# Kernel optimization log

Measured on AMD Instinct MI355X. Metric: run time of the kernel, lower is better.

The kernel has to match this reference:

```python
import jax, jax.numpy as jnp
import numpy as np

EPS = 1e-8
B, CIN, COUT, T, H, W = 16, 16, 64, 50, 32, 32
K = 3  # cubic kernel

# Surrogate-gradient Heaviside spike: forward = step(mthr > 0),
# backward = sigma * sigmoid'(sigma * mthr) (standard SurrogateHeaviside).
@jax.custom_vjp
def spike_fn(mthr, sigma):
    return (mthr > 0.0).astype(mthr.dtype)

def _spk_fwd(mthr, sigma):
    return spike_fn(mthr, sigma), (mthr, sigma)

def _spk_bwd(res, g):
    mthr, sigma = res
    sig = jax.nn.sigmoid(sigma * mthr)
    dsig = sig * (1.0 - sig)
    return (g * sigma * dsig, jnp.sum(g * mthr * dsig).reshape(sigma.shape))

spike_fn.defvjp(_spk_fwd, _spk_bwd)


def setup_inputs() -> dict:
    key = jax.random.key(0)
    k1, k2, k3 = jax.random.split(key, 3)
    x = jax.random.normal(k1, (B, CIN, T, H, W), dtype=jnp.float32)
    # torch init: normal(mean=0, std=w_init_std*sqrt(1/(in_ch*prod(kernel))))
    w = jax.random.normal(k2, (COUT, CIN, K, K, K), jnp.float32) * np.sqrt(1.0 / (CIN * K * K * K)).astype(np.float32)
    v = jax.random.normal(k3, (COUT, COUT), jnp.float32) * np.sqrt(1.0 / COUT).astype(np.float32)
    beta = jnp.full((1,), 0.85, jnp.float32)       # one_per_layer, constant init, clamped [0,1]
    b = jnp.ones((COUT,), jnp.float32)             # constant init 1.0, clamped >= 0
    sigma = jnp.full((1,), 10.0, jnp.float32)      # surrogate_sigma, 'one' mode
    return {"x": x, "w": w, "v": v, "beta": beta, "b": b, "sigma": sigma}


def reference(x, w, v, beta, b, sigma):
    # conv3d front-end, padding=ceil((k-1)*d/2)=1, then crop to output_shape (no-op here)
    conv_x = jax.lax.conv_general_dilated(
        x, w, window_strides=(1, 1, 1), padding=[(1, 1), (1, 1), (1, 1)],
        dimension_numbers=("NCDHW", "OIDHW", "NCDHW"))
    conv_x = conv_x[:, :, :, :H, :W]  # [B, COUT, T, H, W]

    d = jnp.einsum("abcde,fbcde->af", w, w)          # [COUT, COUT] lateral reset mixing
    norm = jnp.sum(w * w, axis=(1, 2, 3, 4))          # [COUT]
    inv_norm = (1.0 / (norm + EPS))[None, :, None, None]
    bmat = b[None, :, None, None]

    batch = x.shape[0]
    mem0 = jnp.zeros((batch, COUT, H, W), x.dtype)
    spk0 = jnp.zeros_like(mem0)
    conv_seq = jnp.moveaxis(conv_x, 2, 0)             # [T, B, COUT, H, W]

    def step(carry, inp_t):
        mem, spk = carry
        rst = jnp.einsum("bchw,ce->behw", spk, d)                 # lateral reset
        inp = inp_t + jnp.einsum("bchw,ce->behw", spk, v)         # recurrent input
        mem = (mem - rst) * beta + inp * (1.0 - beta)             # leaky soft-reset LIF
        mthr = mem * inv_norm - bmat
        spk = spike_fn(mthr, sigma)
        return (mem, spk), spk

    _, spks = jax.lax.scan(step, (mem0, spk0), conv_seq)
    spk_rec = jnp.moveaxis(spks, 0, 2)                # [B, COUT, T, H, W]

    loss = 0.5 * jnp.mean(spk_rec ** 2)
    denom = jnp.asarray(batch * COUT * H * W, spk_rec.dtype)
    spk_spread_loss = jnp.max(jnp.sum(spk_rec, axis=(0, 1, 3, 4))) / denom
    return spk_rec, loss, spk_spread_loss
```

## Files before the change

### kernel.cpp

```cpp
#include <hip/hip_runtime.h>

#define NB    16
#define NCIN  16
#define NCOUT 64
#define NT    50
#define NH    32
#define NW    32
#define NHW   1024
#define WROW  432


__global__ __launch_bounds__(64) void gram_kernel(const float* __restrict__ w,
                                                  float* __restrict__ dmat,
                                                  float* __restrict__ invn) {
    const int c = blockIdx.x;
    const int e = threadIdx.x;
    const float* wc = w + c * WROW;
    const float* we = w + e * WROW;
    float acc = 0.f;
    for (int k = 0; k < WROW; ++k) acc = fmaf(wc[k], we[k], acc);
    dmat[c * 64 + e] = acc;
    if (c == e) invn[e] = 1.0f / (acc + 1e-8f);
}

#define XROW 35
#define XPLANE (34 * XROW)
#define XTOT (3 * XPLANE)

__global__ __launch_bounds__(256) void conv_kernel(const float* __restrict__ x,
                                                   const float* __restrict__ w,
                                                   float* __restrict__ convo) {
    const int t   = blockIdx.x;
    const int b   = blockIdx.y;
    const int og  = blockIdx.z;
    const int tid = threadIdx.x;

    __shared__ float xt[XTOT];
    __shared__ float wsm[NCIN * 27 * 8];

    for (int i = tid; i < XTOT; i += 256) xt[i] = 0.f;

    for (int i = tid; i < NCIN * 27 * 8; i += 256) {
        int oi = i & 7;
        int r  = i >> 3;
        wsm[i] = w[(og * 8 + oi) * WROW + r];
    }

    const int h  = tid >> 3;
    const int w0 = (tid & 7) << 2;
    const int lbase = (h + 1) * XROW + (w0 + 1);

    bool pv[3];
    pv[0] = (t >= 1);
    pv[1] = true;
    pv[2] = (t <= NT - 2);

    const float4* x4 = (const float4*)x;
    const long gb = ((long)b * NCIN * NT + (t - 1)) * 256 + tid;

    float4 pf[3];
#pragma unroll
    for (int kt = 0; kt < 3; ++kt)
        if (pv[kt]) pf[kt] = x4[gb + kt * 256];

    float acc[8][4];
#pragma unroll
    for (int oi = 0; oi < 8; ++oi)
#pragma unroll
        for (int p = 0; p < 4; ++p) acc[oi][p] = 0.f;

#pragma unroll 1
    for (int c = 0; c < NCIN; ++c) {
        __syncthreads();
#pragma unroll
        for (int kt = 0; kt < 3; ++kt) {
            if (pv[kt]) {
                float* d = &xt[kt * XPLANE + lbase];
                d[0] = pf[kt].x; d[1] = pf[kt].y; d[2] = pf[kt].z; d[3] = pf[kt].w;
            }
        }
        if (c + 1 < NCIN) {
            const long g = gb + (long)(c + 1) * (NT * 256);
#pragma unroll
            for (int kt = 0; kt < 3; ++kt)
                if (pv[kt]) pf[kt] = x4[g + kt * 256];
        }
        __syncthreads();

        const float* wc = &wsm[c * 216];
#pragma unroll
        for (int kt = 0; kt < 3; ++kt) {
#pragma unroll
            for (int kh = 0; kh < 3; ++kh) {
                const float* xp = &xt[kt * XPLANE + (h + kh) * XROW + w0];
                float xv[6];
#pragma unroll
                for (int j = 0; j < 6; ++j) xv[j] = xp[j];
#pragma unroll
                for (int kw = 0; kw < 3; ++kw) {
                    const float4* wq = (const float4*)&wc[(kt * 9 + kh * 3 + kw) * 8];
                    float4 wa = wq[0];
                    float4 wb = wq[1];
                    float wv[8] = {wa.x, wa.y, wa.z, wa.w, wb.x, wb.y, wb.z, wb.w};
#pragma unroll
                    for (int oi = 0; oi < 8; ++oi)
#pragma unroll
                        for (int p = 0; p < 4; ++p)
                            acc[oi][p] = fmaf(wv[oi], xv[kw + p], acc[oi][p]);
                }
            }
        }
    }

    const size_t pxbase = ((size_t)(b * NT + t) * NHW + h * NW + w0) * NCOUT + og * 8;
#pragma unroll
    for (int p = 0; p < 4; ++p) {
        float4 v0 = make_float4(acc[0][p], acc[1][p], acc[2][p], acc[3][p]);
        float4 v1 = make_float4(acc[4][p], acc[5][p], acc[6][p], acc[7][p]);
        float4* dst = (float4*)(convo + pxbase + (size_t)p * NCOUT);
        dst[0] = v0;
        dst[1] = v1;
    }
}

__global__ __launch_bounds__(256) void scan_kernel(const float* __restrict__ convo,
                                                   const float* __restrict__ vmatg,
                                                   const float* __restrict__ betap,
                                                   const float* __restrict__ bp,
                                                   const float* __restrict__ dmatg,
                                                   const float* __restrict__ invng,
                                                   unsigned long long* __restrict__ bits) {
    const int tid  = threadIdx.x;
    const int wv   = (blockIdx.x << 2) + (tid >> 6);
    const int lane = tid & 63;
    const int b  = wv >> 10;
    const int px = wv & 1023;

    const float beta = betap[0];
    const float omb  = 1.0f - beta;
    const float bb   = bp[lane];
    const float inv  = invng[lane];

    float mem = 0.f;
    unsigned long long mask = 0ull;

    const float* cbase = convo + ((size_t)(b * NT) * NHW + px) * NCOUT + lane;
    const size_t bitbase = (size_t)(b * NT) * NHW + px;

    float cv_next = cbase[0];
    for (int t = 0; t < NT; ++t) {
        float cv = cv_next;
        if (t + 1 < NT) cv_next = cbase[(size_t)(t + 1) * NHW * NCOUT];

        float rst = 0.f, vin = 0.f;
        unsigned long long m = mask;
        while (m) {
            int c = __builtin_ctzll(m);
            m &= m - 1;
            rst += dmatg[(c << 6) + lane];
            vin += vmatg[(c << 6) + lane];
        }
        float inp = cv + vin;
        mem  = fmaf(mem - rst, beta, inp * omb);
        float mthr = fmaf(mem, inv, -bb);
        int s = mthr > 0.0f;
        mask = __ballot(s);
        if (lane == 0) bits[bitbase + (size_t)t * NHW] = mask;
    }
}

__global__ __launch_bounds__(256) void count_kernel(const unsigned long long* __restrict__ bits,
                                                    int* __restrict__ cnt) {
    const int t = blockIdx.x;
    int sum = 0;
    for (int i = threadIdx.x; i < NB * NHW; i += 256) {
        int b  = i >> 10;
        int px = i & 1023;
        sum += __popcll(bits[((size_t)(b * NT + t) << 10) + px]);
    }
    __shared__ int sh[4];
#pragma unroll
    for (int off = 32; off > 0; off >>= 1) sum += __shfl_down(sum, off);
    if ((threadIdx.x & 63) == 0) sh[threadIdx.x >> 6] = sum;
    __syncthreads();
    if (threadIdx.x == 0) cnt[t] = sh[0] + sh[1] + sh[2] + sh[3];
}

__global__ __launch_bounds__(256) void unpack_kernel(const unsigned long long* __restrict__ bits,
                                                     float* __restrict__ out) {
    const long long total4 = 13107200;
    const long long stride = (long long)gridDim.x * blockDim.x;
    for (long long i4 = (long long)blockIdx.x * 256 + threadIdx.x; i4 < total4; i4 += stride) {
        long long flat = i4 << 2;
        int hw = (int)(flat & 1023);
        long long r = flat >> 10;
        int t = (int)(r % 50);
        long long r2 = r / 50;
        int o = (int)(r2 & 63);
        int b = (int)(r2 >> 6);
        const unsigned long long* bq = bits + ((long long)(b * NT + t) << 10) + hw;
        float4 v;
        v.x = (float)((bq[0] >> o) & 1ull);
        v.y = (float)((bq[1] >> o) & 1ull);
        v.z = (float)((bq[2] >> o) & 1ull);
        v.w = (float)((bq[3] >> o) & 1ull);
        *(float4*)(out + flat) = v;
    }
}

__global__ __launch_bounds__(64) void finalize_kernel(const int* __restrict__ cnt,
                                                      float* __restrict__ out) {
    const int lane = threadIdx.x;
    int c = (lane < NT) ? cnt[lane] : 0;
    int tot = c, mx = c;
#pragma unroll
    for (int off = 32; off > 0; off >>= 1) {
        tot += __shfl_down(tot, off);
        mx = max(mx, __shfl_down(mx, off));
    }
    if (lane == 0) {
        out[52428800] = 0.5f * (float)tot / 52428800.0f;
        out[52428801] = (float)mx / 1048576.0f;
    }
}

extern "C" void kernel_launch(void* const* d_in, const int* in_sizes, int n_in,
                              void* d_out, int out_size, void* d_ws, size_t ws_size,
                              hipStream_t stream) {
    const float* x    = (const float*)d_in[0];
    const float* w    = (const float*)d_in[1];
    const float* v    = (const float*)d_in[2];
    const float* beta = (const float*)d_in[3];
    const float* b    = (const float*)d_in[4];
    float* out = (float*)d_out;

    char* ws = (char*)d_ws;
    float* convo              = (float*)(ws);
    float* dmat               = (float*)(ws + 209715200);
    float* invn               = (float*)(ws + 209715200 + 16384);
    unsigned long long* bits  = (unsigned long long*)(ws + 209731840);
    int* cnt                  = (int*)(ws + 216285440);

    gram_kernel<<<64, 64, 0, stream>>>(w, dmat, invn);
    conv_kernel<<<dim3(NT, NB, 8), 256, 0, stream>>>(x, w, convo);
    scan_kernel<<<4096, 256, 0, stream>>>(convo, v, beta, b, dmat, invn, bits);
    count_kernel<<<NT, 256, 0, stream>>>(bits, cnt);
    unpack_kernel<<<4096, 256, 0, stream>>>(bits, out);
    finalize_kernel<<<1, 64, 0, stream>>>(cnt, out);
}
```

Measured before the change: 613.8 us.

## Double-buffer conv input slab in LDS and reorder grid for x reuse

The conv kernel now keeps two shared-memory copies of the three-plane input slab. The next channel is written into the spare buffer while the current one is computed, which cuts the barriers per channel from two to one. The grid is reordered so the eight output-channel groups for the same (t, b) run as adjacent blocks, which should improve L2 reuse of x. In exchange, shared memory per block roughly doubles for the slab, which may lower occupancy.

```diff
diff --git a/kernel.cpp b/kernel.cpp
--- a/kernel.cpp
+++ b/kernel.cpp
@@ -30,15 +30,28 @@
 __global__ __launch_bounds__(256) void conv_kernel(const float* __restrict__ x,
                                                    const float* __restrict__ w,
                                                    float* __restrict__ convo) {
-    const int t   = blockIdx.x;
-    const int b   = blockIdx.y;
-    const int og  = blockIdx.z;
+    const int og  = blockIdx.x;
+    const int t   = blockIdx.y;
+    const int b   = blockIdx.z;
     const int tid = threadIdx.x;
 
-    __shared__ float xt[XTOT];
+    __shared__ float xt[2][XTOT];
     __shared__ float wsm[NCIN * 27 * 8];
 
-    for (int i = tid; i < XTOT; i += 256) xt[i] = 0.f;
+    bool pv[3];
+    pv[0] = (t >= 1);
+    pv[1] = true;
+    pv[2] = (t <= NT - 2);
+
+    const float4* x4 = (const float4*)x;
+    const long gb = ((long)b * NCIN * NT + (t - 1)) * 256 + tid;
+
+    float4 pf[3];
+#pragma unroll
+    for (int kt = 0; kt < 3; ++kt)
+        if (pv[kt]) pf[kt] = x4[gb + kt * 256];
+
+    for (int i = tid; i < XTOT; i += 256) { xt[0][i] = 0.f; xt[1][i] = 0.f; }
 
     for (int i = tid; i < NCIN * 27 * 8; i += 256) {
         int oi = i & 7;
@@ -50,18 +63,18 @@
     const int w0 = (tid & 7) << 2;
     const int lbase = (h + 1) * XROW + (w0 + 1);
 
-    bool pv[3];
-    pv[0] = (t >= 1);
-    pv[1] = true;
-    pv[2] = (t <= NT - 2);
-
-    const float4* x4 = (const float4*)x;
-    const long gb = ((long)b * NCIN * NT + (t - 1)) * 256 + tid;
-
-    float4 pf[3];
+    __syncthreads();
+
+#pragma unroll
+    for (int kt = 0; kt < 3; ++kt) {
+        if (pv[kt]) {
+            float* d = &xt[0][kt * XPLANE + lbase];
+            d[0] = pf[kt].x; d[1] = pf[kt].y; d[2] = pf[kt].z; d[3] = pf[kt].w;
+        }
+    }
 #pragma unroll
     for (int kt = 0; kt < 3; ++kt)
-        if (pv[kt]) pf[kt] = x4[gb + kt * 256];
+        if (pv[kt]) pf[kt] = x4[gb + (long)(NT * 256) + kt * 256];
 
     float acc[8][4];
 #pragma unroll
@@ -69,47 +82,58 @@
 #pragma unroll
         for (int p = 0; p < 4; ++p) acc[oi][p] = 0.f;
 
+    __syncthreads();
+
+    int cur = 0;
 #pragma unroll 1
     for (int c = 0; c < NCIN; ++c) {
-        __syncthreads();
-#pragma unroll
-        for (int kt = 0; kt < 3; ++kt) {
-            if (pv[kt]) {
-                float* d = &xt[kt * XPLANE + lbase];
-                d[0] = pf[kt].x; d[1] = pf[kt].y; d[2] = pf[kt].z; d[3] = pf[kt].w;
-            }
-        }
         if (c + 1 < NCIN) {
-            const long g = gb + (long)(c + 1) * (NT * 256);
-#pragma unroll
-            for (int kt = 0; kt < 3; ++kt)
-                if (pv[kt]) pf[kt] = x4[g + kt * 256];
-        }
-        __syncthreads();
-
-        const float* wc = &wsm[c * 216];
-#pragma unroll
-        for (int kt = 0; kt < 3; ++kt) {
-#pragma unroll
-            for (int kh = 0; kh < 3; ++kh) {
-                const float* xp = &xt[kt * XPLANE + (h + kh) * XROW + w0];
-                float xv[6];
-#pragma unroll
-                for (int j = 0; j < 6; ++j) xv[j] = xp[j];
-#pragma unroll
-                for (int kw = 0; kw < 3; ++kw) {
-                    const float4* wq = (const float4*)&wc[(kt * 9 + kh * 3 + kw) * 8];
-                    float4 wa = wq[0];
-                    float4 wb = wq[1];
-                    float wv[8] = {wa.x, wa.y, wa.z, wa.w, wb.x, wb.y, wb.z, wb.w};
-#pragma unroll
-                    for (int oi = 0; oi < 8; ++oi)
-#pragma unroll
-                        for (int p = 0; p < 4; ++p)
-                            acc[oi][p] = fmaf(wv[oi], xv[kw + p], acc[oi][p]);
+#pragma unroll
+            for (int kt = 0; kt < 3; ++kt) {
+                if (pv[kt]) {
+                    float* d = &xt[cur ^ 1][kt * XPLANE + lbase];
+                    d[0] = pf[kt].x; d[1] = pf[kt].y; d[2] = pf[kt].z; d[3] = pf[kt].w;
                 }
             }
-        }
+            if (c + 2 < NCIN) {
+                const long g = gb + (long)(c + 2) * (NT * 256);
+#pragma unroll
+                for (int kt = 0; kt < 3; ++kt)
+                    if (pv[kt]) pf[kt] = x4[g + kt * 256];
+            }
+        }
+
+        const float* slab = &xt[cur][0];
+        const float* wc = &wsm[c * 216];
+#pragma unroll
+        for (int kt = 0; kt < 3; ++kt) {
+#pragma unroll
+            for (int kh = 0; kh < 3; ++kh) {
+                const float* xp = &slab[kt * XPLANE + (h + kh) * XROW + w0];
+                float xv[6];
+#pragma unroll
+                for (int j = 0; j < 6; ++j) xv[j] = xp[j];
+#pragma unroll
+                for (int kw = 0; kw < 3; ++kw) {
+                    const float4 wa = *(const float4*)&wc[(kt * 9 + kh * 3 + kw) * 8];
+                    const float4 wb = *(const float4*)&wc[(kt * 9 + kh * 3 + kw) * 8 + 4];
+#pragma unroll
+                    for (int p = 0; p < 4; ++p) {
+                        acc[0][p] = fmaf(wa.x, xv[kw + p], acc[0][p]);
+                        acc[1][p] = fmaf(wa.y, xv[kw + p], acc[1][p]);
+                        acc[2][p] = fmaf(wa.z, xv[kw + p], acc[2][p]);
+                        acc[3][p] = fmaf(wa.w, xv[kw + p], acc[3][p]);
+                        acc[4][p] = fmaf(wb.x, xv[kw + p], acc[4][p]);
+                        acc[5][p] = fmaf(wb.y, xv[kw + p], acc[5][p]);
+                        acc[6][p] = fmaf(wb.z, xv[kw + p], acc[6][p]);
+                        acc[7][p] = fmaf(wb.w, xv[kw + p], acc[7][p]);
+                    }
+                }
+            }
+        }
+
+        __syncthreads();
+        cur ^= 1;
     }
 
     const size_t pxbase = ((size_t)(b * NT + t) * NHW + h * NW + w0) * NCOUT + og * 8;
@@ -242,7 +266,7 @@
     int* cnt                  = (int*)(ws + 216285440);
 
     gram_kernel<<<64, 64, 0, stream>>>(w, dmat, invn);
-    conv_kernel<<<dim3(NT, NB, 8), 256, 0, stream>>>(x, w, convo);
+    conv_kernel<<<dim3(8, NT, NB), 256, 0, stream>>>(x, w, convo);
     scan_kernel<<<4096, 256, 0, stream>>>(convo, v, beta, b, dmat, invn, bits);
     count_kernel<<<NT, 256, 0, stream>>>(bits, cnt);
     unpack_kernel<<<4096, 256, 0, stream>>>(bits, out);
```

Measured after the change: 631.9 us. 1.03x slower.

## Read conv weights from pre-transposed global buffer and vectorize LDS tile loads

Applied to the files above, without the earlier changes.

Adds a small kernel that transposes the weights to [r][cout] layout once, so the conv kernel reads weights as uniform scalar global loads instead of staging them in shared memory. The input tile row pitch goes from 35 to 36 floats so each thread's six-value window can be read as one float4 plus one float2 from LDS. The grid is reordered so the 8 output-channel groups of one (t,b) sit next to each other and share the same x slab in L2. The cost is an extra launch and reliance on scalar cache hits for the weight loads inside the inner loop.

```diff
diff --git a/kernel.cpp b/kernel.cpp
--- a/kernel.cpp
+++ b/kernel.cpp
@@ -23,32 +23,27 @@
     if (c == e) invn[e] = 1.0f / (acc + 1e-8f);
 }
 
-#define XROW 35
+__global__ __launch_bounds__(256) void wtrans_kernel(const float* __restrict__ w,
+                                                     float* __restrict__ wT) {
+    int idx = blockIdx.x * 256 + threadIdx.x;
+    int r = idx >> 6;
+    int o = idx & 63;
+    wT[idx] = w[o * WROW + r];
+}
+
+#define XROW 36
 #define XPLANE (34 * XROW)
 #define XTOT (3 * XPLANE)
 
 __global__ __launch_bounds__(256) void conv_kernel(const float* __restrict__ x,
-                                                   const float* __restrict__ w,
+                                                   const float* __restrict__ wT,
                                                    float* __restrict__ convo) {
-    const int t   = blockIdx.x;
-    const int b   = blockIdx.y;
-    const int og  = blockIdx.z;
+    const int og  = blockIdx.x;
+    const int t   = blockIdx.y;
+    const int b   = blockIdx.z;
     const int tid = threadIdx.x;
 
-    __shared__ float xt[XTOT];
-    __shared__ float wsm[NCIN * 27 * 8];
-
-    for (int i = tid; i < XTOT; i += 256) xt[i] = 0.f;
-
-    for (int i = tid; i < NCIN * 27 * 8; i += 256) {
-        int oi = i & 7;
-        int r  = i >> 3;
-        wsm[i] = w[(og * 8 + oi) * WROW + r];
-    }
-
-    const int h  = tid >> 3;
-    const int w0 = (tid & 7) << 2;
-    const int lbase = (h + 1) * XROW + (w0 + 1);
+    __shared__ __align__(16) float xt[XTOT];
 
     bool pv[3];
     pv[0] = (t >= 1);
@@ -63,15 +58,24 @@
     for (int kt = 0; kt < 3; ++kt)
         if (pv[kt]) pf[kt] = x4[gb + kt * 256];
 
+    for (int i = tid; i < XTOT; i += 256) xt[i] = 0.f;
+
+    const int h  = tid >> 3;
+    const int w0 = (tid & 7) << 2;
+    const int lbase = (h + 1) * XROW + (w0 + 1);
+
+    const float* wtg = wT + og * 8;
+
     float acc[8][4];
 #pragma unroll
     for (int oi = 0; oi < 8; ++oi)
 #pragma unroll
         for (int p = 0; p < 4; ++p) acc[oi][p] = 0.f;
+
+    __syncthreads();
 
 #pragma unroll 1
     for (int c = 0; c < NCIN; ++c) {
-        __syncthreads();
 #pragma unroll
         for (int kt = 0; kt < 3; ++kt) {
             if (pv[kt]) {
@@ -87,29 +91,29 @@
         }
         __syncthreads();
 
-        const float* wc = &wsm[c * 216];
 #pragma unroll
         for (int kt = 0; kt < 3; ++kt) {
 #pragma unroll
             for (int kh = 0; kh < 3; ++kh) {
                 const float* xp = &xt[kt * XPLANE + (h + kh) * XROW + w0];
-                float xv[6];
-#pragma unroll
-                for (int j = 0; j < 6; ++j) xv[j] = xp[j];
+                const float4 xa = *(const float4*)xp;
+                const float2 xb = *(const float2*)(xp + 4);
+                const float xv[6] = {xa.x, xa.y, xa.z, xa.w, xb.x, xb.y};
 #pragma unroll
                 for (int kw = 0; kw < 3; ++kw) {
-                    const float4* wq = (const float4*)&wc[(kt * 9 + kh * 3 + kw) * 8];
-                    float4 wa = wq[0];
-                    float4 wb = wq[1];
-                    float wv[8] = {wa.x, wa.y, wa.z, wa.w, wb.x, wb.y, wb.z, wb.w};
-#pragma unroll
-                    for (int oi = 0; oi < 8; ++oi)
+                    const float* wrow = wtg + (c * 27 + kt * 9 + kh * 3 + kw) * 64;
+#pragma unroll
+                    for (int oi = 0; oi < 8; ++oi) {
+                        const float wv = wrow[oi];
 #pragma unroll
                         for (int p = 0; p < 4; ++p)
-                            acc[oi][p] = fmaf(wv[oi], xv[kw + p], acc[oi][p]);
+                            acc[oi][p] = fmaf(wv, xv[kw + p], acc[oi][p]);
+                    }
                 }
             }
         }
+
+        __syncthreads();
     }
 
     const size_t pxbase = ((size_t)(b * NT + t) * NHW + h * NW + w0) * NCOUT + og * 8;
@@ -240,9 +244,11 @@
     float* invn               = (float*)(ws + 209715200 + 16384);
     unsigned long long* bits  = (unsigned long long*)(ws + 209731840);
     int* cnt                  = (int*)(ws + 216285440);
+    float* wT                 = (float*)(ws + 216285696);
 
     gram_kernel<<<64, 64, 0, stream>>>(w, dmat, invn);
-    conv_kernel<<<dim3(NT, NB, 8), 256, 0, stream>>>(x, w, convo);
+    wtrans_kernel<<<108, 256, 0, stream>>>(w, wT);
+    conv_kernel<<<dim3(8, NT, NB), 256, 0, stream>>>(x, wT, convo);
     scan_kernel<<<4096, 256, 0, stream>>>(convo, v, beta, b, dmat, invn, bits);
     count_kernel<<<NT, 256, 0, stream>>>(bits, cnt);
     unpack_kernel<<<4096, 256, 0, stream>>>(bits, out);
```

Result: faster. 545.3 us (-11.2%).
